# Optimization experiments

Hardware: AMD Instinct MI355X
Metric: run time of the kernel (lower is better)

The kernel has to match this reference:

```python
import jax, jax.numpy as jnp
import numpy as np
from jax import lax

NUM_ITER = 20
STOP_THRESH = 1e-4
# kernels baked from anisotropy=(1,1,0.5): (3,3,3) and (max(1,int(3*s)),...)=(3,3,1)
KERNELS = ((3, 3, 3), (3, 3, 1))
LEAK = 0.01


def _maxpool3d(x, k):
    # x: [B,C,D,H,W]; stride 1, torch-style padding (k-1)//2 (pads with -inf for max)
    window = (1, 1) + k
    pad = [(0, 0), (0, 0)] + [((ki - 1) // 2, (ki - 1) // 2) for ki in k]
    return lax.reduce_window(x, -jnp.inf, lax.max, window, (1,) * 5, pad)


def soft_erode(img):
    p = [-_maxpool3d(-img, k) for k in KERNELS]
    return jnp.minimum(p[0], p[1])


def soft_dilate(img):
    p = [_maxpool3d(img, k) for k in KERNELS]
    return jnp.maximum(p[0], p[1])


def soft_open(img):
    return soft_dilate(soft_erode(img))


def _leaky(x):
    return jax.nn.leaky_relu(x, LEAK)


def soft_skel(img):
    skel = _leaky(img - soft_open(img))
    prev_skel = jnp.zeros_like(skel)
    active = jnp.array(True)  # emulates the data-dependent `break`
    for i in range(NUM_ITER):
        img = soft_erode(img)
        lr = 0.1 * 0.5 ** (i // (NUM_ITER // 5))
        delta = _leaky(img - soft_open(img))
        skel_update = _leaky(delta - skel * delta) * lr
        skel_new = skel + skel_update
        delta_norm = jnp.mean(jnp.abs(skel_new - prev_skel))
        # torch updates skel, THEN checks and breaks; freeze after stop triggers
        skel = jnp.where(active, skel_new, skel)
        active = jnp.logical_and(active, delta_norm >= STOP_THRESH)
        prev_skel = skel
    return skel


def distance_transform(x):
    binary = (x > 0).astype(x.dtype)
    return -1.0 * (1.0 - binary) * _maxpool3d(-binary, (3, 3, 3))


def setup_inputs() -> dict:
    key = jax.random.key(0)
    img = jax.random.uniform(key, (2, 1, 128, 256, 256), dtype=jnp.float32)
    return {"img": img}


def reference(img):
    skel = soft_skel(img)
    dt = distance_transform(lax.stop_gradient(skel))  # mirrors skel.detach()
    return skel * (1.0 + 0.2 * jax.nn.sigmoid(dt))
```

## Files before the change

kernel.cpp:

```cpp
#include <hip/hip_runtime.h>
#include <cmath>

#define D_ 128
#define H_ 256
#define W4 64
#define PS (H_*W4)
#define NTOT (2*128*256*256)
#define GBLK 2048
#define ROWS 8
#define STOPF 1e-4f

typedef _Float16 h4 __attribute__((ext_vector_type(4)));
typedef _Float16 h2v __attribute__((ext_vector_type(2)));

__device__ __forceinline__ float lk(float x){ return x >= 0.f ? x : 0.01f*x; }
__device__ __forceinline__ float4 mn4(float4 a, float4 b){
    return make_float4(fminf(a.x,b.x),fminf(a.y,b.y),fminf(a.z,b.z),fminf(a.w,b.w)); }
__device__ __forceinline__ float4 ld4(const float4* p){ return *p; }
__device__ __forceinline__ float4 ld4(const h4* p){
    h4 v = *p; return make_float4((float)v.x,(float)v.y,(float)v.z,(float)v.w); }
__device__ __forceinline__ void st4(h4* p, float4 v){
    h4 r; r.x=(_Float16)v.x; r.y=(_Float16)v.y; r.z=(_Float16)v.z; r.w=(_Float16)v.w; *p = r; }

#define PINF 0x7C007C00u
#define NINF 0xFC00FC00u
__device__ __forceinline__ uint32_t pmin(uint32_t a, uint32_t b){
    h2v r = __builtin_elementwise_min(__builtin_bit_cast(h2v,a), __builtin_bit_cast(h2v,b));
    return __builtin_bit_cast(uint32_t, r); }
__device__ __forceinline__ uint32_t pmax(uint32_t a, uint32_t b){
    h2v r = __builtin_elementwise_max(__builtin_bit_cast(h2v,a), __builtin_bit_cast(h2v,b));
    return __builtin_bit_cast(uint32_t, r); }
__device__ __forceinline__ uint2 pmin2(uint2 a, uint2 b){
    return make_uint2(pmin(a.x,b.x), pmin(a.y,b.y)); }
__device__ __forceinline__ uint2 pmax2(uint2 a, uint2 b){
    return make_uint2(pmax(a.x,b.x), pmax(a.y,b.y)); }
__device__ __forceinline__ float4 cvt4(uint32_t w01, uint32_t w23){
    h2v a = __builtin_bit_cast(h2v, w01);
    h2v b = __builtin_bit_cast(h2v, w23);
    return make_float4((float)a.x, (float)a.y, (float)b.x, (float)b.y); }

struct Geo { int lane, h0; size_t pbase; bool pm, pp; };
__device__ __forceinline__ Geo mkgeo(int tid, int bi){
    Geo g;
    g.lane = tid & 63;
    int wv = tid >> 6;
    int q = bi & 7, d = (bi >> 3) & 127, b = bi >> 10;
    g.h0 = q*32 + wv*ROWS;
    g.pbase = ((size_t)(b*128 + d))*PS + (size_t)g.lane;
    g.pm = (d > 0); g.pp = (d < 127);
    return g;
}

__device__ __forceinline__ void phase_f32_erode(
    const float4* __restrict__ Xm, const float4* __restrict__ Xc, const float4* __restrict__ Xp,
    bool pm, bool pp, h4* __restrict__ Ep, int h0, int lane)
{
    const float INF = __builtin_inff();
    float4 dmn[3];
    auto ldrow = [&](int j){
        int s = j % 3; int h = h0 - 1 + j;
        if (h >= 0 && h < H_){
            float4 v = ld4(Xc + h*W4); float4 mn = v;
            if (pm){ mn = mn4(mn, ld4(Xm + h*W4)); }
            if (pp){ mn = mn4(mn, ld4(Xp + h*W4)); }
            dmn[s] = mn;
        } else dmn[s] = make_float4(INF,INF,INF,INF);
    };
    ldrow(0); ldrow(1);
#pragma unroll
    for (int r = 0; r < ROWS; ++r){
        ldrow(r+2);
        float4 vmn = mn4(dmn[0], mn4(dmn[1], dmn[2]));
        float lmn = __shfl_up(vmn.w,1);   if (lane == 0)  lmn = INF;
        float rmn = __shfl_down(vmn.x,1); if (lane == 63) rmn = INF;
        float4 e;
        e.x = fminf(lmn,  fminf(vmn.x,vmn.y));
        e.y = fminf(vmn.x,fminf(vmn.y,vmn.z));
        e.z = fminf(vmn.y,fminf(vmn.z,vmn.w));
        e.w = fminf(vmn.z,fminf(vmn.w,rmn));
        st4(Ep + (h0+r)*W4, e);
    }
}

template<int MODE, typename CT>
__device__ __forceinline__ double phase_pk(
    const uint2* __restrict__ Xm, const uint2* __restrict__ Xc, const uint2* __restrict__ Xp,
    bool pm, bool pp,
    uint2* __restrict__ Ep, const CT* __restrict__ Cp, h4* __restrict__ Sp,
    float lr, int h0, int lane)
{
    uint2 rmn[4], rmx[4];
    double loc = 0.0;
    auto ldrow = [&](int j){
        int s = j & 3; int h = h0 - 1 + j;
        if (h >= 0 && h < H_){
            uint2 v = *(Xc + h*W4); uint2 mn = v, mx = v;
            if (pm){ uint2 u = *(Xm + h*W4); mn = pmin2(mn,u); mx = pmax2(mx,u); }
            if (pp){ uint2 u = *(Xp + h*W4); mn = pmin2(mn,u); mx = pmax2(mx,u); }
            rmn[s] = mn; rmx[s] = mx;
        } else {
            rmn[s] = make_uint2(PINF,PINF);
            rmx[s] = make_uint2(NINF,NINF);
        }
    };
    ldrow(0); ldrow(1); ldrow(2);
    float4 a_cur = ld4(Cp + h0*W4);
    float4 s_cur = make_float4(0,0,0,0);
    if constexpr(MODE >= 2) s_cur = ld4(Sp + h0*W4);
#pragma unroll
    for (int r = 0; r < ROWS; ++r){
        if (r + 3 <= ROWS + 1) ldrow(r+3);
        float4 a_nxt = a_cur, s_nxt = s_cur;
        if (r + 1 < ROWS){
            a_nxt = ld4(Cp + (h0+r+1)*W4);
            if constexpr(MODE >= 2) s_nxt = ld4(Sp + (h0+r+1)*W4);
        }
        uint2 vmn = pmin2(rmn[r&3], pmin2(rmn[(r+1)&3], rmn[(r+2)&3]));
        uint2 vmx = pmax2(rmx[r&3], pmax2(rmx[(r+1)&3], rmx[(r+2)&3]));
        uint32_t pwn = __shfl_up(vmn.y,1);   if (lane == 0)  pwn = PINF;
        uint32_t nwn = __shfl_down(vmn.x,1); if (lane == 63) nwn = PINF;
        uint32_t l01 = (pwn  >> 16) | (vmn.x << 16);
        uint32_t l23 = (vmn.x >> 16) | (vmn.y << 16);
        uint32_t r23 = (vmn.y >> 16) | (nwn  << 16);
        uint32_t e01 = pmin(pmin(l01, vmn.x), l23);
        uint32_t e23 = pmin(pmin(l23, vmn.y), r23);
        *(Ep + (h0+r)*W4) = make_uint2(e01, e23);
        uint32_t pwx = __shfl_up(vmx.y,1);   if (lane == 0)  pwx = NINF;
        uint32_t nwx = __shfl_down(vmx.x,1); if (lane == 63) nwx = NINF;
        uint32_t L01 = (pwx  >> 16) | (vmx.x << 16);
        uint32_t L23 = (vmx.x >> 16) | (vmx.y << 16);
        uint32_t R23 = (vmx.y >> 16) | (nwx  << 16);
        uint32_t o01 = pmax(pmax(L01, vmx.x), L23);
        uint32_t o23 = pmax(pmax(L23, vmx.y), R23);
        float4 o = cvt4(o01, o23);
        float4 a = a_cur;
        if constexpr(MODE == 1){
            float4 s0;
            s0.x = lk(a.x-o.x); s0.y = lk(a.y-o.y);
            s0.z = lk(a.z-o.z); s0.w = lk(a.w-o.w);
            st4(Sp + (h0+r)*W4, s0);
        } else {
            float4 s = s_cur;
            float4 up; float dl;
            dl = lk(a.x-o.x); up.x = lk(dl - s.x*dl)*lr; s.x += up.x;
            dl = lk(a.y-o.y); up.y = lk(dl - s.y*dl)*lr; s.y += up.y;
            dl = lk(a.z-o.z); up.z = lk(dl - s.z*dl)*lr; s.z += up.z;
            dl = lk(a.w-o.w); up.w = lk(dl - s.w*dl)*lr; s.w += up.w;
            st4(Sp + (h0+r)*W4, s);
            if constexpr(MODE == 2)
                loc += (double)(fabsf(s.x)+fabsf(s.y)+fabsf(s.z)+fabsf(s.w));
            else
                loc += (double)(fabsf(up.x)+fabsf(up.y)+fabsf(up.z)+fabsf(up.w));
        }
        a_cur = a_nxt; s_cur = s_nxt;
    }
    return loc;
}

__global__ __launch_bounds__(256) void p0_k(const float* __restrict__ img0,
                                            h4* __restrict__ R0,
                                            int* __restrict__ frozen){
    if (blockIdx.x == 0 && threadIdx.x == 0) *frozen = 0;
    Geo g = mkgeo(threadIdx.x, blockIdx.x);
    const float4* Xc = (const float4*)img0 + g.pbase;
    phase_f32_erode(Xc-PS, Xc, Xc+PS, g.pm, g.pp, R0+g.pbase, g.h0, g.lane);
}

__global__ __launch_bounds__(256) void p1_k(const h4* __restrict__ R0,
                                            const float* __restrict__ img0,
                                            h4* __restrict__ R1,
                                            h4* __restrict__ S){
    Geo g = mkgeo(threadIdx.x, blockIdx.x);
    const uint2* Xc = (const uint2*)R0 + g.pbase;
    phase_pk<1,float4>(Xc-PS, Xc, Xc+PS, g.pm, g.pp, (uint2*)R1 + g.pbase,
                       (const float4*)img0 + g.pbase, S + g.pbase, 0.f, g.h0, g.lane);
}

template<int MODE>
__global__ __launch_bounds__(256) void upd_k(const h4* __restrict__ Xb,
                                             const h4* __restrict__ Cb,
                                             h4* __restrict__ Eb,
                                             h4* __restrict__ Sb,
                                             const double* __restrict__ pr,
                                             double* __restrict__ pw,
                                             int* __restrict__ frozen,
                                             float lr){
    if (*frozen) return;
    __shared__ double sm[4];
    int tid = threadIdx.x;
    int lane = tid & 63, wv = tid >> 6;
    if constexpr(MODE == 3){
        double v = 0.0;
#pragma unroll
        for (int j = 0; j < GBLK/256; ++j) v += pr[tid + 256*j];
#pragma unroll
        for (int o = 32; o; o >>= 1) v += __shfl_down(v, o);
        if (lane == 0) sm[wv] = v;
        __syncthreads();
        double tot = sm[0] + sm[1] + sm[2] + sm[3];
        if ((float)(tot / (double)NTOT) < STOPF){
            if (tid == 0) *frozen = 1;
            return;
        }
        __syncthreads();
    }
    Geo g = mkgeo(tid, blockIdx.x);
    const uint2* Xc = (const uint2*)Xb + g.pbase;
    double loc = phase_pk<MODE,h4>(Xc-PS, Xc, Xc+PS, g.pm, g.pp,
                                   (uint2*)Eb + g.pbase, Cb + g.pbase, Sb + g.pbase,
                                   lr, g.h0, g.lane);
#pragma unroll
    for (int o = 32; o; o >>= 1) loc += __shfl_down(loc, o);
    if (lane == 0) sm[wv] = loc;
    __syncthreads();
    if (tid == 0) pw[blockIdx.x] = sm[0]+sm[1]+sm[2]+sm[3];
}

__global__ __launch_bounds__(256) void scale_k(const h4* __restrict__ S,
                                               float* __restrict__ out){
    int t = blockIdx.x*256 + threadIdx.x;
#pragma unroll
    for (int c = 0; c < 4; ++c){
        int i = t + c*1048576;
        float4 s = ld4(S + i);
        float4 r = make_float4(1.1f*s.x, 1.1f*s.y, 1.1f*s.z, 1.1f*s.w);
        *(float4*)(out + (size_t)i*4) = r;
    }
}

extern "C" void kernel_launch(void* const* d_in, const int* in_sizes, int n_in,
                              void* d_out, int out_size, void* d_ws, size_t ws_size,
                              hipStream_t stream){
    const float* img0 = (const float*)d_in[0];
    float* out = (float*)d_out;
    char* ws = (char*)d_ws;
    size_t volh = (size_t)NTOT * 2;
    h4* ring[3] = { (h4*)ws, (h4*)(ws + volh), (h4*)(ws + 2*volh) };
    h4* S       = (h4*)(ws + 3*volh);
    double* parts[2] = { (double*)(ws + 4*volh), (double*)(ws + 4*volh) + GBLK };
    int* frozen = (int*)(ws + 4*volh + 2*GBLK*sizeof(double));

    dim3 blk(256), grd(GBLK);
    hipLaunchKernelGGL(p0_k, grd, blk, 0, stream, img0, ring[0], frozen);
    hipLaunchKernelGGL(p1_k, grd, blk, 0, stream, ring[0], img0, ring[1], S);

    for (int i = 0; i < 20; ++i){
        h4* C = ring[i % 3];
        h4* X = ring[(i+1) % 3];
        h4* E = ring[(i+2) % 3];
        float lr = (float)(0.1 * pow(0.5, (double)(i / 4)));
        double* pw = parts[i & 1];
        double* pr = parts[1 - (i & 1)];
        if (i == 0)
            hipLaunchKernelGGL((upd_k<2>), grd, blk, 0, stream, X, C, E, S, pr, pw, frozen, lr);
        else
            hipLaunchKernelGGL((upd_k<3>), grd, blk, 0, stream, X, C, E, S, pr, pw, frozen, lr);
    }
    hipLaunchKernelGGL(scale_k, dim3(4096), blk, 0, stream, S, out);
}
```

Before: 292.9 us.

## Run later skeleton iterations in one persistent cooperative kernel with grid sync

Iterations from index 6 onward move into a single cooperative kernel of 1024 blocks that loops, reduces the per-block partial norms itself and uses a grid-wide sync between iterations. This removes a kernel launch per iteration and lets the early-stop path write the scaled output directly, replacing the separate scale pass. The erosion prologue also gains a four-slot row ring with one extra row of prefetch. In exchange each thread handles 16 rows instead of 8 and every iteration pays a grid barrier, with a fallback to per-iteration launches if the cooperative launch fails.

New measurement: 289.7 us. About the same (-1.1%).

```diff
diff --git a/kernel.cpp b/kernel.cpp
--- a/kernel.cpp
+++ b/kernel.cpp
@@ -1,4 +1,5 @@
 #include <hip/hip_runtime.h>
+#include <hip/hip_cooperative_groups.h>
 #include <cmath>
 
 #define D_ 128
@@ -8,6 +9,7 @@
 #define NTOT (2*128*256*256)
 #define GBLK 2048
 #define ROWS 8
+#define TSTART 6
 #define STOPF 1e-4f
 
 typedef _Float16 h4 __attribute__((ext_vector_type(4)));
@@ -21,6 +23,8 @@
     h4 v = *p; return make_float4((float)v.x,(float)v.y,(float)v.z,(float)v.w); }
 __device__ __forceinline__ void st4(h4* p, float4 v){
     h4 r; r.x=(_Float16)v.x; r.y=(_Float16)v.y; r.z=(_Float16)v.z; r.w=(_Float16)v.w; *p = r; }
+__device__ __forceinline__ float4 h4tof4(h4 v){
+    return make_float4((float)v.x,(float)v.y,(float)v.z,(float)v.w); }
 
 #define PINF 0x7C007C00u
 #define NINF 0xFC00FC00u
@@ -56,9 +60,9 @@
     bool pm, bool pp, h4* __restrict__ Ep, int h0, int lane)
 {
     const float INF = __builtin_inff();
-    float4 dmn[3];
+    float4 dmn[4];
     auto ldrow = [&](int j){
-        int s = j % 3; int h = h0 - 1 + j;
+        int s = j & 3; int h = h0 - 1 + j;
         if (h >= 0 && h < H_){
             float4 v = ld4(Xc + h*W4); float4 mn = v;
             if (pm){ mn = mn4(mn, ld4(Xm + h*W4)); }
@@ -66,11 +70,11 @@
             dmn[s] = mn;
         } else dmn[s] = make_float4(INF,INF,INF,INF);
     };
-    ldrow(0); ldrow(1);
+    ldrow(0); ldrow(1); ldrow(2);
 #pragma unroll
     for (int r = 0; r < ROWS; ++r){
-        ldrow(r+2);
-        float4 vmn = mn4(dmn[0], mn4(dmn[1], dmn[2]));
+        if (r + 3 <= ROWS + 1) ldrow(r+3);
+        float4 vmn = mn4(dmn[r&3], mn4(dmn[(r+1)&3], dmn[(r+2)&3]));
         float lmn = __shfl_up(vmn.w,1);   if (lane == 0)  lmn = INF;
         float rmn = __shfl_down(vmn.x,1); if (lane == 63) rmn = INF;
         float4 e;
@@ -82,7 +86,7 @@
     }
 }
 
-template<int MODE, typename CT>
+template<int MODE, int R, typename CT>
 __device__ __forceinline__ double phase_pk(
     const uint2* __restrict__ Xm, const uint2* __restrict__ Xc, const uint2* __restrict__ Xp,
     bool pm, bool pp,
@@ -108,10 +112,10 @@
     float4 s_cur = make_float4(0,0,0,0);
     if constexpr(MODE >= 2) s_cur = ld4(Sp + h0*W4);
 #pragma unroll
-    for (int r = 0; r < ROWS; ++r){
-        if (r + 3 <= ROWS + 1) ldrow(r+3);
+    for (int r = 0; r < R; ++r){
+        if (r + 3 <= R + 1) ldrow(r+3);
         float4 a_nxt = a_cur, s_nxt = s_cur;
-        if (r + 1 < ROWS){
+        if (r + 1 < R){
             a_nxt = ld4(Cp + (h0+r+1)*W4);
             if constexpr(MODE >= 2) s_nxt = ld4(Sp + (h0+r+1)*W4);
         }
@@ -172,8 +176,8 @@
                                             h4* __restrict__ S){
     Geo g = mkgeo(threadIdx.x, blockIdx.x);
     const uint2* Xc = (const uint2*)R0 + g.pbase;
-    phase_pk<1,float4>(Xc-PS, Xc, Xc+PS, g.pm, g.pp, (uint2*)R1 + g.pbase,
-                       (const float4*)img0 + g.pbase, S + g.pbase, 0.f, g.h0, g.lane);
+    phase_pk<1,ROWS,float4>(Xc-PS, Xc, Xc+PS, g.pm, g.pp, (uint2*)R1 + g.pbase,
+                            (const float4*)img0 + g.pbase, S + g.pbase, 0.f, g.h0, g.lane);
 }
 
 template<int MODE>
@@ -184,6 +188,7 @@
                                              const double* __restrict__ pr,
                                              double* __restrict__ pw,
                                              int* __restrict__ frozen,
+                                             float* __restrict__ outp,
                                              float lr){
     if (*frozen) return;
     __shared__ double sm[4];
@@ -200,20 +205,84 @@
         double tot = sm[0] + sm[1] + sm[2] + sm[3];
         if ((float)(tot / (double)NTOT) < STOPF){
             if (tid == 0) *frozen = 1;
+            Geo g = mkgeo(tid, blockIdx.x);
+            const h4* Sp = Sb + g.pbase;
+            float4* O = (float4*)outp + g.pbase;
+#pragma unroll
+            for (int r = 0; r < ROWS; ++r){
+                float4 s = h4tof4(Sp[(g.h0+r)*W4]);
+                O[(g.h0+r)*W4] = make_float4(1.1f*s.x, 1.1f*s.y, 1.1f*s.z, 1.1f*s.w);
+            }
             return;
         }
         __syncthreads();
     }
     Geo g = mkgeo(tid, blockIdx.x);
     const uint2* Xc = (const uint2*)Xb + g.pbase;
-    double loc = phase_pk<MODE,h4>(Xc-PS, Xc, Xc+PS, g.pm, g.pp,
-                                   (uint2*)Eb + g.pbase, Cb + g.pbase, Sb + g.pbase,
-                                   lr, g.h0, g.lane);
+    double loc = phase_pk<MODE,ROWS,h4>(Xc-PS, Xc, Xc+PS, g.pm, g.pp,
+                                        (uint2*)Eb + g.pbase, Cb + g.pbase, Sb + g.pbase,
+                                        lr, g.h0, g.lane);
 #pragma unroll
     for (int o = 32; o; o >>= 1) loc += __shfl_down(loc, o);
     if (lane == 0) sm[wv] = loc;
     __syncthreads();
     if (tid == 0) pw[blockIdx.x] = sm[0]+sm[1]+sm[2]+sm[3];
+}
+
+__global__ __launch_bounds__(256) void tail_k(h4* __restrict__ rg0,
+                                              h4* __restrict__ rg1,
+                                              h4* __restrict__ rg2,
+                                              h4* __restrict__ S,
+                                              float* __restrict__ outp,
+                                              const double* __restrict__ pr0,
+                                              double* __restrict__ tp0,
+                                              double* __restrict__ tp1,
+                                              const int* __restrict__ frozen){
+    if (*frozen) return;
+    cooperative_groups::grid_group gg = cooperative_groups::this_grid();
+    __shared__ double sm[4];
+    int tid = threadIdx.x, lane = tid & 63, wv = tid >> 6;
+    int bi = blockIdx.x;
+    int d = bi >> 3, b = (bi >> 2) & 1, q = bi & 3;
+    int h0 = q*64 + wv*16;
+    size_t pbase = ((size_t)(b*128 + d))*PS + (size_t)lane;
+    bool pm = d > 0, pp = d < 127;
+    const double* pr = pr0; int prn = GBLK;
+    double* tpw = tp0;
+    for (int i = TSTART; i < 20; ++i){
+        double v = 0.0;
+        for (int j = 0; j < prn/256; ++j) v += pr[tid + 256*j];
+#pragma unroll
+        for (int o = 32; o; o >>= 1) v += __shfl_down(v, o);
+        if (lane == 0) sm[wv] = v;
+        __syncthreads();
+        double tot = sm[0] + sm[1] + sm[2] + sm[3];
+        if ((float)(tot / (double)NTOT) < STOPF) break;
+        __syncthreads();
+        int xs = (i+1)%3, es = (i+2)%3, cs = i%3;
+        h4* X = xs==0 ? rg0 : (xs==1 ? rg1 : rg2);
+        h4* E = es==0 ? rg0 : (es==1 ? rg1 : rg2);
+        h4* C = cs==0 ? rg0 : (cs==1 ? rg1 : rg2);
+        float lr = 0.1f * exp2f(-(float)(i >> 2));
+        const uint2* Xc = (const uint2*)X + pbase;
+        double loc = phase_pk<3,16,h4>(Xc-PS, Xc, Xc+PS, pm, pp, (uint2*)E + pbase,
+                                       C + pbase, S + pbase, lr, h0, lane);
+#pragma unroll
+        for (int o = 32; o; o >>= 1) loc += __shfl_down(loc, o);
+        if (lane == 0) sm[wv] = loc;
+        __syncthreads();
+        if (tid == 0) tpw[blockIdx.x] = sm[0]+sm[1]+sm[2]+sm[3];
+        gg.sync();
+        pr = tpw; prn = 1024;
+        tpw = (tpw == tp0) ? tp1 : tp0;
+    }
+    const h4* Sp = S + pbase;
+    float4* O = (float4*)outp + pbase;
+#pragma unroll
+    for (int r = 0; r < 16; ++r){
+        float4 s = h4tof4(Sp[(h0+r)*W4]);
+        O[(h0+r)*W4] = make_float4(1.1f*s.x, 1.1f*s.y, 1.1f*s.z, 1.1f*s.w);
+    }
 }
 
 __global__ __launch_bounds__(256) void scale_k(const h4* __restrict__ S,
@@ -239,12 +308,14 @@
     h4* S       = (h4*)(ws + 3*volh);
     double* parts[2] = { (double*)(ws + 4*volh), (double*)(ws + 4*volh) + GBLK };
     int* frozen = (int*)(ws + 4*volh + 2*GBLK*sizeof(double));
+    double* tp0 = (double*)(ws + 4*volh + 2*GBLK*sizeof(double) + 256);
+    double* tp1 = tp0 + 1024;
 
     dim3 blk(256), grd(GBLK);
     hipLaunchKernelGGL(p0_k, grd, blk, 0, stream, img0, ring[0], frozen);
     hipLaunchKernelGGL(p1_k, grd, blk, 0, stream, ring[0], img0, ring[1], S);
 
-    for (int i = 0; i < 20; ++i){
+    for (int i = 0; i < TSTART; ++i){
         h4* C = ring[i % 3];
         h4* X = ring[(i+1) % 3];
         h4* E = ring[(i+2) % 3];
@@ -252,9 +323,28 @@
         double* pw = parts[i & 1];
         double* pr = parts[1 - (i & 1)];
         if (i == 0)
-            hipLaunchKernelGGL((upd_k<2>), grd, blk, 0, stream, X, C, E, S, pr, pw, frozen, lr);
+            hipLaunchKernelGGL((upd_k<2>), grd, blk, 0, stream, X, C, E, S, pr, pw, frozen, out, lr);
         else
-            hipLaunchKernelGGL((upd_k<3>), grd, blk, 0, stream, X, C, E, S, pr, pw, frozen, lr);
-    }
-    hipLaunchKernelGGL(scale_k, dim3(4096), blk, 0, stream, S, out);
-}
+            hipLaunchKernelGGL((upd_k<3>), grd, blk, 0, stream, X, C, E, S, pr, pw, frozen, out, lr);
+    }
+
+    h4* a_r0 = ring[0]; h4* a_r1 = ring[1]; h4* a_r2 = ring[2];
+    h4* a_S = S; float* a_out = out;
+    const double* a_pr0 = parts[1 - (TSTART & 1)];
+    double* a_tp0 = tp0; double* a_tp1 = tp1; int* a_fz = frozen;
+    void* args[9] = { &a_r0, &a_r1, &a_r2, &a_S, &a_out, &a_pr0, &a_tp0, &a_tp1, &a_fz };
+    hipError_t ce = hipLaunchCooperativeKernel((const void*)tail_k, dim3(1024), blk,
+                                               args, 0u, stream);
+    if (ce != hipSuccess){
+        for (int i = TSTART; i < 20; ++i){
+            h4* C = ring[i % 3];
+            h4* X = ring[(i+1) % 3];
+            h4* E = ring[(i+2) % 3];
+            float lr = (float)(0.1 * pow(0.5, (double)(i / 4)));
+            double* pw = parts[i & 1];
+            double* pr = parts[1 - (i & 1)];
+            hipLaunchKernelGGL((upd_k<3>), grd, blk, 0, stream, X, C, E, S, pr, pw, frozen, out, lr);
+        }
+        hipLaunchKernelGGL(scale_k, dim3(4096), blk, 0, stream, S, out);
+    }
+}
```
